# Optimization experiments

Measured on AMD Instinct MI355X. Metric: run time of the kernel, lower is better.

## Reference

```python
import jax, jax.numpy as jnp
import numpy as np


def setup_inputs() -> dict:
    key = jax.random.key(0)
    k = jax.random.split(key, 5)
    bs, n_heads, ch, n_obj, emb = 4, 8, 64, 8, 64
    ih = iw = 32
    T = ih * iw
    return {
        "qkv": jax.random.normal(k[0], (bs, 3 * n_heads * ch, T), dtype=jnp.float32),
        "bboxes": jax.random.uniform(k[1], (bs, n_obj, 5), dtype=jnp.float32),
        "null_prompt_emb": jax.random.normal(k[2], (bs, emb, T), dtype=jnp.float32),
        "prompt_emb": jax.random.normal(k[3], (bs, emb, T), dtype=jnp.float32),
        "W_prompt": jax.random.normal(k[4], (3 * n_heads * ch, emb), dtype=jnp.float32) * 0.02,
        "n_heads": n_heads,
        "image_h": ih,
        "image_w": iw,
    }


def _region_masks(bboxes, h, w):
    # Faithful translation of get_region: bbox unpacked as (x, y, width, height, obj_idx).
    # Returns float masks [b, n_obj, h*w].
    x, y, bw, bh = bboxes[..., 0], bboxes[..., 1], bboxes[..., 2], bboxes[..., 3]
    i0 = jnp.minimum(float(h) - 1.0, jnp.floor(y * h))
    j0 = jnp.minimum(float(w) - 1.0, jnp.floor(x * w))
    i1 = i0 + jnp.maximum(1.0, jnp.ceil(bh * h))
    j1 = j0 + jnp.maximum(1.0, jnp.ceil(bw * w))
    ii = jnp.arange(h, dtype=jnp.float32)
    jj = jnp.arange(w, dtype=jnp.float32)
    mi = (ii >= i0[..., None]) & (ii < i1[..., None])          # [b, n, h]
    mj = (jj >= j0[..., None]) & (jj < j1[..., None])          # [b, n, w]
    m = (mi[..., :, None] & mj[..., None, :]).astype(jnp.float32)  # [b, n, h, w]
    return m.reshape(m.shape[0], m.shape[1], h * w)


def reference(qkv, bboxes, null_prompt_emb, prompt_emb, W_prompt, n_heads, image_h, image_w):
    bs, width, T = qkv.shape
    ch = width // (3 * n_heads)
    scale = float(ch) ** -0.25  # 1/sqrt(sqrt(ch))

    def split3(x):
        x = x.reshape(bs * n_heads, 3 * ch, T)
        return x[:, :ch], x[:, ch:2 * ch], x[:, 2 * ch:]

    q, k, v = split3(qkv)
    # to_prompt_token is a 1x1 Conv1d (no bias) == matmul over the channel dim
    nq, nk, nv = split3(jnp.einsum('oc,bct->bot', W_prompt, null_prompt_emb))
    pq, pk, pv = split3(jnp.einsum('oc,bct->bot', W_prompt, prompt_emb))

    def attn(qh, kh, vh, col_mask=None):
        w = jnp.einsum('bct,bcs->bts', qh * scale, kh * scale)
        if col_mask is not None:
            w = jnp.where(col_mask[:, None, :] > 0.5, w, -1e9)
        w = jax.nn.softmax(w.astype(jnp.float32), axis=-1).astype(qh.dtype)
        return jnp.einsum('bts,bcs->btc', w, vh)  # [bs*heads, T, ch]

    # global (null-prompt) attention
    a_null = attn(q + nq, k + nk, v + nv)

    # per-object masked attention, blended by region masks
    masks = _region_masks(bboxes, image_h, image_w)       # [bs, n_obj, T]
    masks = jnp.repeat(masks, n_heads, axis=0)            # [(bs*heads), n_obj, T]
    qf, kf, vf = q + pq, k + pk, v + pv
    a_fg = jnp.zeros_like(a_null)
    counter = jnp.zeros((bs * n_heads, T, 1), dtype=jnp.float32)
    for o in range(masks.shape[1]):  # small fixed loop over objects
        m = masks[:, o]                                   # [bs*heads, T]
        a_fg = a_fg + m[:, :, None] * attn(qf, kf, vf, col_mask=m)
        counter = counter + m[:, :, None]
    fg = counter > 0.5
    a_final = jnp.where(fg, a_fg, a_null) / jnp.where(fg, counter, 1.0)
    return jnp.transpose(a_final, (0, 2, 1)).reshape(bs, n_heads * ch, T)
```

## Files before the change

kernel.cpp:

```cpp
#include <hip/hip_runtime.h>
#include <math.h>

#define BS 4
#define NH 8
#define TT 1024
#define WROWS 1536
#define NOBJ 8
#define NT 65536

#define QNT_OFF  0
#define KNT_OFF  2097152
#define VNCS_OFF 4194304
#define QFT_OFF  6291456
#define KFT_OFF  8388608
#define VFT_OFF  10485760

typedef __attribute__((ext_vector_type(8))) short short8;
typedef __attribute__((ext_vector_type(4))) float v4f;

#if __has_builtin(__builtin_amdgcn_exp2f)
#define EXP2(x) __builtin_amdgcn_exp2f(x)
#else
#define EXP2(x) exp2f(x)
#endif

__device__ __forceinline__ short f2bf(float f) {
    unsigned u = __float_as_uint(f);
    u = (u + 0x7FFF + ((u >> 16) & 1)) >> 16;
    return (short)u;
}
__device__ __forceinline__ unsigned p2(float a, float b) {
    return (unsigned)(unsigned short)f2bf(a) | ((unsigned)(unsigned short)f2bf(b) << 16);
}
__device__ __forceinline__ unsigned p2t(float a, float b) {
    return (__float_as_uint(a) >> 16) | (__float_as_uint(b) & 0xFFFF0000u);
}

__device__ __forceinline__ void get_region(const float* __restrict__ bb,
                                           int& i0, int& j0, int& hh, int& ww) {
    float x = bb[0], y = bb[1], bw = bb[2], bh = bb[3];
    float i0f = fminf(31.0f, floorf(y * 32.0f));
    float j0f = fminf(31.0f, floorf(x * 32.0f));
    float i1f = i0f + fmaxf(1.0f, ceilf(bh * 32.0f));
    float j1f = j0f + fmaxf(1.0f, ceilf(bw * 32.0f));
    i0 = (int)i0f; j0 = (int)j0f;
    int i1 = min(32, (int)i1f);
    int j1 = min(32, (int)j1f);
    hh = i1 - i0; ww = j1 - j0;
}

__global__ __launch_bounds__(256)
void fuse_kernel(const float* __restrict__ qkv, const float* __restrict__ nEmb,
                 const float* __restrict__ pEmb, const float* __restrict__ W,
                 short* __restrict__ wsS) {
    __shared__ float WtT[64][68];
    __shared__ float En[64][64];
    __shared__ float Ep[64][64];
    short* sbufA = (short*)&WtT[0][0];
    short* sbufB = (short*)&En[0][0];
    int t0 = blockIdx.x * 64;
    int r0 = blockIdx.y * 64;
    int b  = blockIdx.z;
    int tid = threadIdx.x;
    int half = tid >> 4;
    int q4 = (tid & 15) * 4;
    int tr = tid >> 4, tc = tid & 15;
    float4 xq[4];
#pragma unroll
    for (int i = 0; i < 4; ++i)
        xq[i] = *(const float4*)&qkv[(b * WROWS + r0 + tr * 4 + i) * TT + t0 + tc * 4];
#pragma unroll
    for (int p = 0; p < 4; ++p) {
        int rr = p * 16 + half;
        float4 w4 = *(const float4*)&W[(r0 + rr) * 64 + q4];
        WtT[q4 + 0][rr] = w4.x; WtT[q4 + 1][rr] = w4.y;
        WtT[q4 + 2][rr] = w4.z; WtT[q4 + 3][rr] = w4.w;
        int e = p * 16 + half;
        *(float4*)&En[e][q4] = *(const float4*)&nEmb[(b * 64 + e) * TT + t0 + q4];
        *(float4*)&Ep[e][q4] = *(const float4*)&pEmb[(b * 64 + e) * TT + t0 + q4];
    }
    __syncthreads();
    float an[4][4] = {{0.f}}, ap[4][4] = {{0.f}};
#pragma unroll 8
    for (int e = 0; e < 64; ++e) {
        float4 w4 = *(const float4*)&WtT[e][tr * 4];
        float4 n4 = *(const float4*)&En[e][tc * 4];
        float4 p4 = *(const float4*)&Ep[e][tc * 4];
        float w[4]  = {w4.x, w4.y, w4.z, w4.w};
        float nn[4] = {n4.x, n4.y, n4.z, n4.w};
        float pp[4] = {p4.x, p4.y, p4.z, p4.w};
#pragma unroll
        for (int i = 0; i < 4; ++i)
#pragma unroll
            for (int j = 0; j < 4; ++j) {
                an[i][j] += w[i] * nn[j];
                ap[i][j] += w[i] * pp[j];
            }
    }
    int sec = (r0 % 192) / 64;
    int h = r0 / 192, bh = b * 8 + h;
    float sc = (sec == 0) ? 0.18033688f : 1.0f;
#pragma unroll
    for (int i = 0; i < 4; ++i) {
        float4 x4 = xq[i];
        an[i][0] = (an[i][0] + x4.x) * sc; an[i][1] = (an[i][1] + x4.y) * sc;
        an[i][2] = (an[i][2] + x4.z) * sc; an[i][3] = (an[i][3] + x4.w) * sc;
        ap[i][0] = (ap[i][0] + x4.x) * sc; ap[i][1] = (ap[i][1] + x4.y) * sc;
        ap[i][2] = (ap[i][2] + x4.z) * sc; ap[i][3] = (ap[i][3] + x4.w) * sc;
    }
    if (sec == 2) {
        short* Vn = wsS + VNCS_OFF + bh * NT;
#pragma unroll
        for (int i = 0; i < 4; ++i) {
            int c = tr * 4 + i;
            uint2 pk; pk.x = p2(an[i][0], an[i][1]); pk.y = p2(an[i][2], an[i][3]);
            *(uint2*)&Vn[c * TT + t0 + tc * 4] = pk;
        }
        short* dst = wsS + VFT_OFF + bh * NT + t0 * 64;
        __syncthreads();
#pragma unroll
        for (int i = 0; i < 4; ++i)
#pragma unroll
            for (int j = 0; j < 4; ++j)
                sbufB[(tc * 4 + j) * 72 + tr * 4 + i] = f2bf(ap[i][j]);
        __syncthreads();
#pragma unroll
        for (int rep = 0; rep < 2; ++rep) {
            int idx = rep * 256 + tid; int tl = idx >> 3, c8 = idx & 7;
            *(short8*)&dst[tl * 64 + c8 * 8] = *(const short8*)&sbufB[tl * 72 + c8 * 8];
        }
    } else {
        short* dn = wsS + (sec == 0 ? QNT_OFF : KNT_OFF) + bh * NT + t0 * 64;
        short* df = wsS + (sec == 0 ? QFT_OFF : KFT_OFF) + bh * NT + t0 * 64;
        __syncthreads();
#pragma unroll
        for (int i = 0; i < 4; ++i)
#pragma unroll
            for (int j = 0; j < 4; ++j) {
                sbufA[(tc * 4 + j) * 72 + tr * 4 + i] = f2bf(an[i][j]);
                sbufB[(tc * 4 + j) * 72 + tr * 4 + i] = f2bf(ap[i][j]);
            }
        __syncthreads();
#pragma unroll
        for (int rep = 0; rep < 2; ++rep) {
            int idx = rep * 256 + tid; int tl = idx >> 3, c8 = idx & 7;
            *(short8*)&dn[tl * 64 + c8 * 8] = *(const short8*)&sbufA[tl * 72 + c8 * 8];
            *(short8*)&df[tl * 64 + c8 * 8] = *(const short8*)&sbufB[tl * 72 + c8 * 8];
        }
    }
}

__global__ __launch_bounds__(256)
void attn_fused(const short* __restrict__ wsS, const float* __restrict__ bboxes,
                float* __restrict__ out) {
    __shared__ __align__(16) short lds[13824];
    __shared__ unsigned short tmap[1024];
    short* Qs = lds;
    short* Ks = lds + 4608;
    short* Vs = lds + 9216;
    int bh = blockIdx.x, rt = blockIdx.y;
    int b = bh >> 3, h = bh & 7;
    int t0 = rt * 64;
    int tid = threadIdx.x;
    int w = tid >> 6, lane = tid & 63, ln = lane & 15, qd = lane >> 4;
    const short* QnT = wsS + QNT_OFF + bh * NT;
    const short* KnT = wsS + KNT_OFF + bh * NT;
    const short* Vn  = wsS + VNCS_OFF + bh * NT;
    const short* QfT = wsS + QFT_OFF + bh * NT;
    const short* KfT = wsS + KFT_OFF + bh * NT;
    const short* VfT = wsS + VFT_OFF + bh * NT;

    int r0i = 2 * rt, r1i = 2 * rt + 1;
    unsigned inter = 0u, cov0 = 0u, cov1 = 0u;
    for (int o = 0; o < NOBJ; ++o) {
        int i0, j0, hh, ww;
        get_region(&bboxes[(b * NOBJ + o) * 5], i0, j0, hh, ww);
        int i1 = i0 + hh;
        if (i0 <= r1i && i1 > r0i) {
            inter |= (1u << o);
            unsigned wm = (ww >= 32) ? 0xFFFFFFFFu : (((1u << ww) - 1u) << j0);
            if (i0 <= r0i && r0i < i1) cov0 |= wm;
            if (i0 <= r1i && r1i < i1) cov1 |= wm;
        }
    }

    v4f Onull[4];
#pragma unroll
    for (int cc = 0; cc < 4; ++cc) Onull[cc] = (v4f){0.f, 0.f, 0.f, 0.f};

    if ((cov0 & cov1) != 0xFFFFFFFFu) {
#pragma unroll
        for (int rep = 0; rep < 2; ++rep) {
            int idx = rep * 256 + tid; int cell = idx >> 3, o8 = idx & 7;
            *(short8*)&Qs[cell * 72 + o8 * 8] =
                *(const short8*)&QnT[(t0 + cell) * 64 + o8 * 8];
        }
        __syncthreads();
        short8 aq0 = *(const short8*)&Qs[(16 * w + ln) * 72 + qd * 8];
        short8 aq1 = *(const short8*)&Qs[(16 * w + ln) * 72 + 32 + qd * 8];
        v4f O[4]; float l[4];
#pragma unroll
        for (int r = 0; r < 4; ++r) l[r] = 0.f;
#pragma unroll
        for (int cc = 0; cc < 4; ++cc) O[cc] = (v4f){0.f, 0.f, 0.f, 0.f};
        short8 kreg[2], vreg[2];
#pragma unroll
        for (int rep = 0; rep < 2; ++rep) {
            int idx = rep * 256 + tid; int cell = idx >> 3, o8 = idx & 7;
            int pc = 4 * (cell & 15) + (cell >> 4);
            kreg[rep] = *(const short8*)&KnT[pc * 64 + o8 * 8];
            vreg[rep] = *(const short8*)&Vn[cell * TT + o8 * 8];
        }
        for (int ct = 0; ct < 16; ++ct) {
            __syncthreads();
#pragma unroll
            for (int rep = 0; rep < 2; ++rep) {
                int idx = rep * 256 + tid; int cell = idx >> 3, o8 = idx & 7;
                *(short8*)&Ks[cell * 72 + o8 * 8] = kreg[rep];
                *(short8*)&Vs[cell * 72 + o8 * 8] = vreg[rep];
            }
            __syncthreads();
            if (ct < 15) {
                int s0 = (ct + 1) * 64;
#pragma unroll
                for (int rep = 0; rep < 2; ++rep) {
                    int idx = rep * 256 + tid; int cell = idx >> 3, o8 = idx & 7;
                    int pc = 4 * (cell & 15) + (cell >> 4);
                    kreg[rep] = *(const short8*)&KnT[(s0 + pc) * 64 + o8 * 8];
                    vreg[rep] = *(const short8*)&Vn[cell * TT + s0 + o8 * 8];
                }
            }
            v4f S[4];
#pragma unroll
            for (int nn = 0; nn < 4; ++nn) {
                short8 b0 = *(const short8*)&Ks[(nn * 16 + ln) * 72 + qd * 8];
                short8 b1 = *(const short8*)&Ks[(nn * 16 + ln) * 72 + 32 + qd * 8];
                v4f z = (v4f){0.f, 0.f, 0.f, 0.f};
                z = __builtin_amdgcn_mfma_f32_16x16x32_bf16(aq0, b0, z, 0, 0, 0);
                z = __builtin_amdgcn_mfma_f32_16x16x32_bf16(aq1, b1, z, 0, 0, 0);
                S[nn] = z;
            }
#pragma unroll
            for (int r = 0; r < 4; ++r) {
                float e0 = EXP2(S[0][r]);
                float e1 = EXP2(S[1][r]);
                float e2 = EXP2(S[2][r]);
                float e3 = EXP2(S[3][r]);
                l[r] += e0 + e1 + e2 + e3;
                uint2 pk; pk.x = p2t(e0, e1); pk.y = p2t(e2, e3);
                *(uint2*)&Qs[(w * 16 + 4 * qd + r) * 72 + 4 * ln] = pk;
            }
            short8 ap0 = *(const short8*)&Qs[(w * 16 + ln) * 72 + qd * 8];
            short8 ap1 = *(const short8*)&Qs[(w * 16 + ln) * 72 + 32 + qd * 8];
#pragma unroll
            for (int cc = 0; cc < 4; ++cc) {
                short8 bv0 = *(const short8*)&Vs[(cc * 16 + ln) * 72 + qd * 8];
                short8 bv1 = *(const short8*)&Vs[(cc * 16 + ln) * 72 + 32 + qd * 8];
                O[cc] = __builtin_amdgcn_mfma_f32_16x16x32_bf16(ap0, bv0, O[cc], 0, 0, 0);
                O[cc] = __builtin_amdgcn_mfma_f32_16x16x32_bf16(ap1, bv1, O[cc], 0, 0, 0);
            }
        }
#pragma unroll
        for (int r = 0; r < 4; ++r) {
            float rs = l[r];
            rs += __shfl_xor(rs, 1, 64);
            rs += __shfl_xor(rs, 2, 64);
            rs += __shfl_xor(rs, 4, 64);
            rs += __shfl_xor(rs, 8, 64);
            float inv = 1.0f / rs;
#pragma unroll
            for (int cc = 0; cc < 4; ++cc) Onull[cc][r] = O[cc][r] * inv;
        }
    }

    v4f Oacc[4]; float cnt[4];
#pragma unroll
    for (int r = 0; r < 4; ++r) cnt[r] = 0.f;
#pragma unroll
    for (int cc = 0; cc < 4; ++cc) Oacc[cc] = (v4f){0.f, 0.f, 0.f, 0.f};

    if (inter != 0u) {
        __syncthreads();
#pragma unroll
        for (int rep = 0; rep < 2; ++rep) {
            int idx = rep * 256 + tid; int cell = idx >> 3, o8 = idx & 7;
            *(short8*)&Qs[cell * 72 + o8 * 8] =
                *(const short8*)&QfT[(t0 + cell) * 64 + o8 * 8];
        }
        __syncthreads();
        short8 aq0 = *(const short8*)&Qs[(16 * w + ln) * 72 + qd * 8];
        short8 aq1 = *(const short8*)&Qs[(16 * w + ln) * 72 + 32 + qd * 8];
        for (int o = 0; o < NOBJ; ++o) {
            if (!((inter >> o) & 1u)) continue;
            int i0, j0, hh, ww;
            get_region(&bboxes[(b * NOBJ + o) * 5], i0, j0, hh, ww);
            int i1 = i0 + hh;
            int R = hh * ww;
            for (int idx = tid; idx < R; idx += 256) {
                int ri = idx / ww; int rj = idx - ri * ww;
                tmap[idx] = (unsigned short)((i0 + ri) * 32 + j0 + rj);
            }
            __syncthreads();
            v4f O[4]; float l[4];
#pragma unroll
            for (int r = 0; r < 4; ++r) l[r] = 0.f;
#pragma unroll
            for (int cc = 0; cc < 4; ++cc) O[cc] = (v4f){0.f, 0.f, 0.f, 0.f};
            int nct = (R + 63) >> 6;
            short8 kreg[2], vreg[2];
#pragma unroll
            for (int rep = 0; rep < 2; ++rep) {
                int idx = rep * 256 + tid; int cell = idx >> 3, o8 = idx & 7;
                int pc = 4 * (cell & 15) + (cell >> 4);
                int tk = tmap[min(pc, R - 1)];
                int tv = tmap[min(cell, R - 1)];
                kreg[rep] = *(const short8*)&KfT[tk * 64 + o8 * 8];
                vreg[rep] = *(const short8*)&VfT[tv * 64 + o8 * 8];
            }
            for (int ct = 0; ct < nct; ++ct) {
                int sb = ct * 64;
                __syncthreads();
#pragma unroll
                for (int rep = 0; rep < 2; ++rep) {
                    int idx = rep * 256 + tid; int cell = idx >> 3, o8 = idx & 7;
                    *(short8*)&Ks[cell * 72 + o8 * 8] = kreg[rep];
#pragma unroll
                    for (int jj = 0; jj < 8; ++jj) {
                        int j = (jj + o8) & 7;
                        Vs[(o8 * 8 + j) * 72 + cell] = vreg[rep][j];
                    }
                }
                __syncthreads();
                if (ct + 1 < nct) {
                    int s0 = sb + 64;
#pragma unroll
                    for (int rep = 0; rep < 2; ++rep) {
                        int idx = rep * 256 + tid; int cell = idx >> 3, o8 = idx & 7;
                        int pc = 4 * (cell & 15) + (cell >> 4);
                        int tk = tmap[min(s0 + pc, R - 1)];
                        int tv = tmap[min(s0 + cell, R - 1)];
                        kreg[rep] = *(const short8*)&KfT[tk * 64 + o8 * 8];
                        vreg[rep] = *(const short8*)&VfT[tv * 64 + o8 * 8];
                    }
                }
                v4f S[4];
#pragma unroll
                for (int nn = 0; nn < 4; ++nn) {
                    short8 b0 = *(const short8*)&Ks[(nn * 16 + ln) * 72 + qd * 8];
                    short8 b1 = *(const short8*)&Ks[(nn * 16 + ln) * 72 + 32 + qd * 8];
                    v4f z = (v4f){0.f, 0.f, 0.f, 0.f};
                    z = __builtin_amdgcn_mfma_f32_16x16x32_bf16(aq0, b0, z, 0, 0, 0);
                    z = __builtin_amdgcn_mfma_f32_16x16x32_bf16(aq1, b1, z, 0, 0, 0);
                    S[nn] = z;
                }
                float v0 = (sb + 4 * ln + 0) < R ? 1.f : 0.f;
                float v1 = (sb + 4 * ln + 1) < R ? 1.f : 0.f;
                float v2 = (sb + 4 * ln + 2) < R ? 1.f : 0.f;
                float v3 = (sb + 4 * ln + 3) < R ? 1.f : 0.f;
#pragma unroll
                for (int r = 0; r < 4; ++r) {
                    float e0 = EXP2(S[0][r]) * v0;
                    float e1 = EXP2(S[1][r]) * v1;
                    float e2 = EXP2(S[2][r]) * v2;
                    float e3 = EXP2(S[3][r]) * v3;
                    l[r] += e0 + e1 + e2 + e3;
                    uint2 pk; pk.x = p2t(e0, e1); pk.y = p2t(e2, e3);
                    *(uint2*)&Qs[(w * 16 + 4 * qd + r) * 72 + 4 * ln] = pk;
                }
                short8 ap0 = *(const short8*)&Qs[(w * 16 + ln) * 72 + qd * 8];
                short8 ap1 = *(const short8*)&Qs[(w * 16 + ln) * 72 + 32 + qd * 8];
#pragma unroll
                for (int cc = 0; cc < 4; ++cc) {
                    short8 bv0 = *(const short8*)&Vs[(cc * 16 + ln) * 72 + qd * 8];
                    short8 bv1 = *(const short8*)&Vs[(cc * 16 + ln) * 72 + 32 + qd * 8];
                    O[cc] = __builtin_amdgcn_mfma_f32_16x16x32_bf16(ap0, bv0, O[cc], 0, 0, 0);
                    O[cc] = __builtin_amdgcn_mfma_f32_16x16x32_bf16(ap1, bv1, O[cc], 0, 0, 0);
                }
            }
#pragma unroll
            for (int r = 0; r < 4; ++r) {
                float rs = l[r];
                rs += __shfl_xor(rs, 1, 64);
                rs += __shfl_xor(rs, 2, 64);
                rs += __shfl_xor(rs, 4, 64);
                rs += __shfl_xor(rs, 8, 64);
                float inv = 1.0f / rs;
                int t = t0 + 16 * w + 4 * qd + r;
                int ti = t >> 5, tj = t & 31;
                bool in = (ti >= i0) && (ti < i1) && (tj >= j0) && (tj < j0 + ww);
                if (in) {
                    cnt[r] += 1.f;
#pragma unroll
                    for (int cc = 0; cc < 4; ++cc) Oacc[cc][r] += O[cc][r] * inv;
                }
            }
        }
    }

    __syncthreads();
    float* Ot = (float*)lds;
#pragma unroll
    for (int r = 0; r < 4; ++r) {
        int tl = 16 * w + 4 * qd + r;
        float icnt = cnt[r] > 0.f ? 1.0f / cnt[r] : 0.f;
#pragma unroll
        for (int cc = 0; cc < 4; ++cc) {
            float val = cnt[r] > 0.f ? Oacc[cc][r] * icnt : Onull[cc][r];
            Ot[(cc * 16 + ln) * 68 + tl] = val;
        }
    }
    __syncthreads();
    int obase = (b * 512 + h * 64) * TT + t0;
#pragma unroll
    for (int rep = 0; rep < 4; ++rep) {
        int idx = rep * 256 + tid; int c = idx >> 4, t4 = (idx & 15) * 4;
        *(float4*)&out[obase + c * TT + t4] = *(float4*)&Ot[c * 68 + t4];
    }
}

extern "C" void kernel_launch(void* const* d_in, const int* in_sizes, int n_in,
                              void* d_out, int out_size, void* d_ws, size_t ws_size,
                              hipStream_t stream) {
    const float* qkv    = (const float*)d_in[0];
    const float* bboxes = (const float*)d_in[1];
    const float* nEmb   = (const float*)d_in[2];
    const float* pEmb   = (const float*)d_in[3];
    const float* W      = (const float*)d_in[4];
    short* wsS = (short*)d_ws;
    float* out = (float*)d_out;

    fuse_kernel<<<dim3(16, 24, 4), 256, 0, stream>>>(qkv, nEmb, pEmb, W, wsS);
    attn_fused<<<dim3(32, 16), 256, 0, stream>>>(wsS, bboxes, out);
}
```

Before: 162.1 us.

## Compute null attention only for uncovered tokens via compacted token list

Adds a small kernel that builds, per batch, a compacted list of tokens not covered by any bbox. A new kernel runs null-prompt attention only for those query rows, in 16-row tiles with the key range split across four waves and a reduction through shared memory. The foreground kernel no longer computes null attention and writes only covered tokens. This drops null attention for covered rows (previously done for any 64-row tile with an uncovered token), at the cost of two extra launches, scattered output stores and gathered query loads.

```diff
diff --git a/kernel.cpp b/kernel.cpp
--- a/kernel.cpp
+++ b/kernel.cpp
@@ -14,6 +14,8 @@
 #define QFT_OFF  6291456
 #define KFT_OFF  8388608
 #define VFT_OFF  10485760
+#define ULIST_OFF 12582912
+#define UCNT_BYTE_OFF 25174016
 
 typedef __attribute__((ext_vector_type(8))) short short8;
 typedef __attribute__((ext_vector_type(4))) float v4f;
@@ -47,6 +49,48 @@
     int i1 = min(32, (int)i1f);
     int j1 = min(32, (int)j1f);
     hh = i1 - i0; ww = j1 - j0;
+}
+
+__global__ __launch_bounds__(256)
+void list_kernel(const float* __restrict__ bboxes,
+                 unsigned short* __restrict__ ulist, int* __restrict__ ucnt) {
+    int b = blockIdx.x, tid = threadIdx.x;
+    int I0[NOBJ], I1[NOBJ], J0[NOBJ], J1[NOBJ];
+#pragma unroll
+    for (int o = 0; o < NOBJ; ++o) {
+        int i0, j0, hh, ww;
+        get_region(&bboxes[(b * NOBJ + o) * 5], i0, j0, hh, ww);
+        I0[o] = i0; I1[o] = i0 + hh; J0[o] = j0; J1[o] = j0 + ww;
+    }
+    int u[4], uc = 0;
+#pragma unroll
+    for (int j = 0; j < 4; ++j) {
+        int t = tid * 4 + j, ti = t >> 5, tj = t & 31;
+        bool cov = false;
+#pragma unroll
+        for (int o = 0; o < NOBJ; ++o)
+            cov = cov || (ti >= I0[o] && ti < I1[o] && tj >= J0[o] && tj < J1[o]);
+        u[j] = cov ? 0 : 1; uc += u[j];
+    }
+    int lane = tid & 63, w = tid >> 6;
+    int s = uc;
+#pragma unroll
+    for (int d = 1; d < 64; d <<= 1) {
+        int v = __shfl_up(s, d, 64);
+        if (lane >= d) s += v;
+    }
+    __shared__ int wsum[4];
+    if (lane == 63) wsum[w] = s;
+    __syncthreads();
+    int off = 0;
+    for (int i = 0; i < w; ++i) off += wsum[i];
+    int base = off + s - uc;
+    int k = 0;
+#pragma unroll
+    for (int j = 0; j < 4; ++j) {
+        if (u[j]) { ulist[b * 1024 + base + k] = (unsigned short)(tid * 4 + j); ++k; }
+    }
+    if (tid == 0) ucnt[b] = wsum[0] + wsum[1] + wsum[2] + wsum[3];
 }
 
 __global__ __launch_bounds__(256)
@@ -151,8 +195,117 @@
 }
 
 __global__ __launch_bounds__(256)
-void attn_fused(const short* __restrict__ wsS, const float* __restrict__ bboxes,
-                float* __restrict__ out) {
+void attn_null_u(const short* __restrict__ wsS,
+                 const unsigned short* __restrict__ ulist,
+                 const int* __restrict__ ucnt, float* __restrict__ out) {
+    __shared__ __align__(16) short Ps[4 * 1152];
+    __shared__ float Rbuf[3][64][20];
+    int bh = blockIdx.x, rt = blockIdx.y;
+    int b = bh >> 3, h = bh & 7;
+    int U = ucnt[b];
+    int n0 = rt * 16;
+    if (n0 >= U) return;
+    int tid = threadIdx.x;
+    int w = tid >> 6, lane = tid & 63, ln = lane & 15, qd = lane >> 4;
+    const short* QnT = wsS + QNT_OFF + bh * NT;
+    const short* KnT = wsS + KNT_OFF + bh * NT;
+    const short* Vn  = wsS + VNCS_OFF + bh * NT;
+    const unsigned short* ul = ulist + b * 1024;
+    int trow = ul[min(n0 + ln, U - 1)];
+    short8 aq0 = *(const short8*)&QnT[trow * 64 + qd * 8];
+    short8 aq1 = *(const short8*)&QnT[trow * 64 + 32 + qd * 8];
+    v4f O[4]; float l[4];
+#pragma unroll
+    for (int r = 0; r < 4; ++r) l[r] = 0.f;
+#pragma unroll
+    for (int cc = 0; cc < 4; ++cc) O[cc] = (v4f){0.f, 0.f, 0.f, 0.f};
+    short* Pw = Ps + w * 1152;
+#pragma unroll
+    for (int i = 0; i < 4; ++i) {
+        int s0 = (w * 4 + i) * 64;
+        short8 kf[4][2], vf[4][2];
+#pragma unroll
+        for (int nn = 0; nn < 4; ++nn) {
+            int base = (s0 + 4 * ln + nn) * 64;
+            kf[nn][0] = *(const short8*)&KnT[base + qd * 8];
+            kf[nn][1] = *(const short8*)&KnT[base + 32 + qd * 8];
+        }
+#pragma unroll
+        for (int cc = 0; cc < 4; ++cc) {
+            int base = (cc * 16 + ln) * TT + s0;
+            vf[cc][0] = *(const short8*)&Vn[base + qd * 8];
+            vf[cc][1] = *(const short8*)&Vn[base + 32 + qd * 8];
+        }
+        v4f S[4];
+#pragma unroll
+        for (int nn = 0; nn < 4; ++nn) {
+            v4f z = (v4f){0.f, 0.f, 0.f, 0.f};
+            z = __builtin_amdgcn_mfma_f32_16x16x32_bf16(aq0, kf[nn][0], z, 0, 0, 0);
+            z = __builtin_amdgcn_mfma_f32_16x16x32_bf16(aq1, kf[nn][1], z, 0, 0, 0);
+            S[nn] = z;
+        }
+#pragma unroll
+        for (int r = 0; r < 4; ++r) {
+            float e0 = EXP2(S[0][r]);
+            float e1 = EXP2(S[1][r]);
+            float e2 = EXP2(S[2][r]);
+            float e3 = EXP2(S[3][r]);
+            l[r] += e0 + e1 + e2 + e3;
+            uint2 pk; pk.x = p2t(e0, e1); pk.y = p2t(e2, e3);
+            *(uint2*)&Pw[(qd * 4 + r) * 72 + 4 * ln] = pk;
+        }
+        short8 ap0 = *(const short8*)&Pw[ln * 72 + qd * 8];
+        short8 ap1 = *(const short8*)&Pw[ln * 72 + 32 + qd * 8];
+#pragma unroll
+        for (int cc = 0; cc < 4; ++cc) {
+            O[cc] = __builtin_amdgcn_mfma_f32_16x16x32_bf16(ap0, vf[cc][0], O[cc], 0, 0, 0);
+            O[cc] = __builtin_amdgcn_mfma_f32_16x16x32_bf16(ap1, vf[cc][1], O[cc], 0, 0, 0);
+        }
+    }
+#pragma unroll
+    for (int r = 0; r < 4; ++r) {
+        l[r] += __shfl_xor(l[r], 1, 64);
+        l[r] += __shfl_xor(l[r], 2, 64);
+        l[r] += __shfl_xor(l[r], 4, 64);
+        l[r] += __shfl_xor(l[r], 8, 64);
+    }
+    if (w > 0) {
+#pragma unroll
+        for (int cc = 0; cc < 4; ++cc)
+#pragma unroll
+            for (int r = 0; r < 4; ++r) Rbuf[w - 1][lane][cc * 4 + r] = O[cc][r];
+#pragma unroll
+        for (int r = 0; r < 4; ++r) Rbuf[w - 1][lane][16 + r] = l[r];
+    }
+    __syncthreads();
+    if (w == 0) {
+#pragma unroll
+        for (int ww = 0; ww < 3; ++ww) {
+#pragma unroll
+            for (int cc = 0; cc < 4; ++cc)
+#pragma unroll
+                for (int r = 0; r < 4; ++r) O[cc][r] += Rbuf[ww][lane][cc * 4 + r];
+#pragma unroll
+            for (int r = 0; r < 4; ++r) l[r] += Rbuf[ww][lane][16 + r];
+        }
+        int obase = (b * 512 + h * 64) * TT;
+#pragma unroll
+        for (int r = 0; r < 4; ++r) {
+            int rank = n0 + qd * 4 + r;
+            if (rank < U) {
+                int t = ul[rank];
+                float inv = 1.0f / l[r];
+#pragma unroll
+                for (int cc = 0; cc < 4; ++cc)
+                    out[obase + (cc * 16 + ln) * TT + t] = O[cc][r] * inv;
+            }
+        }
+    }
+}
+
+__global__ __launch_bounds__(256)
+void attn_fg(const short* __restrict__ wsS, const float* __restrict__ bboxes,
+             float* __restrict__ out) {
     __shared__ __align__(16) short lds[13824];
     __shared__ unsigned short tmap[1024];
     short* Qs = lds;
@@ -163,9 +316,6 @@
     int t0 = rt * 64;
     int tid = threadIdx.x;
     int w = tid >> 6, lane = tid & 63, ln = lane & 15, qd = lane >> 4;
-    const short* QnT = wsS + QNT_OFF + bh * NT;
-    const short* KnT = wsS + KNT_OFF + bh * NT;
-    const short* Vn  = wsS + VNCS_OFF + bh * NT;
     const short* QfT = wsS + QFT_OFF + bh * NT;
     const short* KfT = wsS + KFT_OFF + bh * NT;
     const short* VfT = wsS + VFT_OFF + bh * NT;
@@ -183,51 +333,74 @@
             if (i0 <= r1i && r1i < i1) cov1 |= wm;
         }
     }
-
-    v4f Onull[4];
-#pragma unroll
-    for (int cc = 0; cc < 4; ++cc) Onull[cc] = (v4f){0.f, 0.f, 0.f, 0.f};
-
-    if ((cov0 & cov1) != 0xFFFFFFFFu) {
-#pragma unroll
-        for (int rep = 0; rep < 2; ++rep) {
-            int idx = rep * 256 + tid; int cell = idx >> 3, o8 = idx & 7;
-            *(short8*)&Qs[cell * 72 + o8 * 8] =
-                *(const short8*)&QnT[(t0 + cell) * 64 + o8 * 8];
+    if (inter == 0u) return;
+
+#pragma unroll
+    for (int rep = 0; rep < 2; ++rep) {
+        int idx = rep * 256 + tid; int cell = idx >> 3, o8 = idx & 7;
+        *(short8*)&Qs[cell * 72 + o8 * 8] =
+            *(const short8*)&QfT[(t0 + cell) * 64 + o8 * 8];
+    }
+    __syncthreads();
+    short8 aq0 = *(const short8*)&Qs[(16 * w + ln) * 72 + qd * 8];
+    short8 aq1 = *(const short8*)&Qs[(16 * w + ln) * 72 + 32 + qd * 8];
+    v4f Oacc[4]; float cnt[4];
+#pragma unroll
+    for (int r = 0; r < 4; ++r) cnt[r] = 0.f;
+#pragma unroll
+    for (int cc = 0; cc < 4; ++cc) Oacc[cc] = (v4f){0.f, 0.f, 0.f, 0.f};
+
+    for (int o = 0; o < NOBJ; ++o) {
+        if (!((inter >> o) & 1u)) continue;
+        int i0, j0, hh, ww;
+        get_region(&bboxes[(b * NOBJ + o) * 5], i0, j0, hh, ww);
+        int i1 = i0 + hh;
+        int R = hh * ww;
+        for (int idx = tid; idx < R; idx += 256) {
+            int ri = idx / ww; int rj = idx - ri * ww;
+            tmap[idx] = (unsigned short)((i0 + ri) * 32 + j0 + rj);
         }
         __syncthreads();
-        short8 aq0 = *(const short8*)&Qs[(16 * w + ln) * 72 + qd * 8];
-        short8 aq1 = *(const short8*)&Qs[(16 * w + ln) * 72 + 32 + qd * 8];
         v4f O[4]; float l[4];
 #pragma unroll
         for (int r = 0; r < 4; ++r) l[r] = 0.f;
 #pragma unroll
         for (int cc = 0; cc < 4; ++cc) O[cc] = (v4f){0.f, 0.f, 0.f, 0.f};
+        int nct = (R + 63) >> 6;
         short8 kreg[2], vreg[2];
 #pragma unroll
         for (int rep = 0; rep < 2; ++rep) {
             int idx = rep * 256 + tid; int cell = idx >> 3, o8 = idx & 7;
             int pc = 4 * (cell & 15) + (cell >> 4);
-            kreg[rep] = *(const short8*)&KnT[pc * 64 + o8 * 8];
-            vreg[rep] = *(const short8*)&Vn[cell * TT + o8 * 8];
-        }
-        for (int ct = 0; ct < 16; ++ct) {
+            int tk = tmap[min(pc, R - 1)];
+            int tv = tmap[min(cell, R - 1)];
+            kreg[rep] = *(const short8*)&KfT[tk * 64 + o8 * 8];
+            vreg[rep] = *(const short8*)&VfT[tv * 64 + o8 * 8];
+        }
+        for (int ct = 0; ct < nct; ++ct) {
+            int sb = ct * 64;
             __syncthreads();
 #pragma unroll
             for (int rep = 0; rep < 2; ++rep) {
                 int idx = rep * 256 + tid; int cell = idx >> 3, o8 = idx & 7;
                 *(short8*)&Ks[cell * 72 + o8 * 8] = kreg[rep];
-                *(short8*)&Vs[cell * 72 + o8 * 8] = vreg[rep];
+#pragma unroll
+                for (int jj = 0; jj < 8; ++jj) {
+                    int j = (jj + o8) & 7;
+                    Vs[(o8 * 8 + j) * 72 + cell] = vreg[rep][j];
+                }
             }
             __syncthreads();
-            if (ct < 15) {
-                int s0 = (ct + 1) * 64;
+            if (ct + 1 < nct) {
+                int s0 = sb + 64;
 #pragma unroll
                 for (int rep = 0; rep < 2; ++rep) {
                     int idx = rep * 256 + tid; int cell = idx >> 3, o8 = idx & 7;
                     int pc = 4 * (cell & 15) + (cell >> 4);
-                    kreg[rep] = *(const short8*)&KnT[(s0 + pc) * 64 + o8 * 8];
-                    vreg[rep] = *(const short8*)&Vn[cell * TT + s0 + o8 * 8];
+                    int tk = tmap[min(s0 + pc, R - 1)];
+                    int tv = tmap[min(s0 + cell, R - 1)];
+                    kreg[rep] = *(const short8*)&KfT[tk * 64 + o8 * 8];
+                    vreg[rep] = *(const short8*)&VfT[tv * 64 + o8 * 8];
                 }
             }
             v4f S[4];
@@ -240,12 +413,16 @@
                 z = __builtin_amdgcn_mfma_f32_16x16x32_bf16(aq1, b1, z, 0, 0, 0);
                 S[nn] = z;
             }
+            float v0 = (sb + 4 * ln + 0) < R ? 1.f : 0.f;
+            float v1 = (sb + 4 * ln + 1) < R ? 1.f : 0.f;
+            float v2 = (sb + 4 * ln + 2) < R ? 1.f : 0.f;
+            float v3 = (sb + 4 * ln + 3) < R ? 1.f : 0.f;
 #pragma unroll
             for (int r = 0; r < 4; ++r) {
-                float e0 = EXP2(S[0][r]);
-                float e1 = EXP2(S[1][r]);
-                float e2 = EXP2(S[2][r]);
-                float e3 = EXP2(S[3][r]);
+                float e0 = EXP2(S[0][r]) * v0;
+                float e1 = EXP2(S[1][r]) * v1;
+                float e2 = EXP2(S[2][r]) * v2;
+                float e3 = EXP2(S[3][r]) * v3;
                 l[r] += e0 + e1 + e2 + e3;
                 uint2 pk; pk.x = p2t(e0, e1); pk.y = p2t(e2, e3);
                 *(uint2*)&Qs[(w * 16 + 4 * qd + r) * 72 + 4 * ln] = pk;
@@ -268,131 +445,13 @@
             rs += __shfl_xor(rs, 4, 64);
             rs += __shfl_xor(rs, 8, 64);
             float inv = 1.0f / rs;
-#pragma unroll
-            for (int cc = 0; cc < 4; ++cc) Onull[cc][r] = O[cc][r] * inv;
-        }
-    }
-
-    v4f Oacc[4]; float cnt[4];
-#pragma unroll
-    for (int r = 0; r < 4; ++r) cnt[r] = 0.f;
-#pragma unroll
-    for (int cc = 0; cc < 4; ++cc) Oacc[cc] = (v4f){0.f, 0.f, 0.f, 0.f};
-
-    if (inter != 0u) {
-        __syncthreads();
-#pragma unroll
-        for (int rep = 0; rep < 2; ++rep) {
-            int idx = rep * 256 + tid; int cell = idx >> 3, o8 = idx & 7;
-            *(short8*)&Qs[cell * 72 + o8 * 8] =
-                *(const short8*)&QfT[(t0 + cell) * 64 + o8 * 8];
-        }
-        __syncthreads();
-        short8 aq0 = *(const short8*)&Qs[(16 * w + ln) * 72 + qd * 8];
-        short8 aq1 = *(const short8*)&Qs[(16 * w + ln) * 72 + 32 + qd * 8];
-        for (int o = 0; o < NOBJ; ++o) {
-            if (!((inter >> o) & 1u)) continue;
-            int i0, j0, hh, ww;
-            get_region(&bboxes[(b * NOBJ + o) * 5], i0, j0, hh, ww);
-            int i1 = i0 + hh;
-            int R = hh * ww;
-            for (int idx = tid; idx < R; idx += 256) {
-                int ri = idx / ww; int rj = idx - ri * ww;
-                tmap[idx] = (unsigned short)((i0 + ri) * 32 + j0 + rj);
-            }
-            __syncthreads();
-            v4f O[4]; float l[4];
-#pragma unroll
-            for (int r = 0; r < 4; ++r) l[r] = 0.f;
-#pragma unroll
-            for (int cc = 0; cc < 4; ++cc) O[cc] = (v4f){0.f, 0.f, 0.f, 0.f};
-            int nct = (R + 63) >> 6;
-            short8 kreg[2], vreg[2];
-#pragma unroll
-            for (int rep = 0; rep < 2; ++rep) {
-                int idx = rep * 256 + tid; int cell = idx >> 3, o8 = idx & 7;
-                int pc = 4 * (cell & 15) + (cell >> 4);
-                int tk = tmap[min(pc, R - 1)];
-                int tv = tmap[min(cell, R - 1)];
-                kreg[rep] = *(const short8*)&KfT[tk * 64 + o8 * 8];
-                vreg[rep] = *(const short8*)&VfT[tv * 64 + o8 * 8];
-            }
-            for (int ct = 0; ct < nct; ++ct) {
-                int sb = ct * 64;
-                __syncthreads();
-#pragma unroll
-                for (int rep = 0; rep < 2; ++rep) {
-                    int idx = rep * 256 + tid; int cell = idx >> 3, o8 = idx & 7;
-                    *(short8*)&Ks[cell * 72 + o8 * 8] = kreg[rep];
-#pragma unroll
-                    for (int jj = 0; jj < 8; ++jj) {
-                        int j = (jj + o8) & 7;
-                        Vs[(o8 * 8 + j) * 72 + cell] = vreg[rep][j];
-                    }
-                }
-                __syncthreads();
-                if (ct + 1 < nct) {
-                    int s0 = sb + 64;
-#pragma unroll
-                    for (int rep = 0; rep < 2; ++rep) {
-                        int idx = rep * 256 + tid; int cell = idx >> 3, o8 = idx & 7;
-                        int pc = 4 * (cell & 15) + (cell >> 4);
-                        int tk = tmap[min(s0 + pc, R - 1)];
-                        int tv = tmap[min(s0 + cell, R - 1)];
-                        kreg[rep] = *(const short8*)&KfT[tk * 64 + o8 * 8];
-                        vreg[rep] = *(const short8*)&VfT[tv * 64 + o8 * 8];
-                    }
-                }
-                v4f S[4];
-#pragma unroll
-                for (int nn = 0; nn < 4; ++nn) {
-                    short8 b0 = *(const short8*)&Ks[(nn * 16 + ln) * 72 + qd * 8];
-                    short8 b1 = *(const short8*)&Ks[(nn * 16 + ln) * 72 + 32 + qd * 8];
-                    v4f z = (v4f){0.f, 0.f, 0.f, 0.f};
-                    z = __builtin_amdgcn_mfma_f32_16x16x32_bf16(aq0, b0, z, 0, 0, 0);
-                    z = __builtin_amdgcn_mfma_f32_16x16x32_bf16(aq1, b1, z, 0, 0, 0);
-                    S[nn] = z;
-                }
-                float v0 = (sb + 4 * ln + 0) < R ? 1.f : 0.f;
-                float v1 = (sb + 4 * ln + 1) < R ? 1.f : 0.f;
-                float v2 = (sb + 4 * ln + 2) < R ? 1.f : 0.f;
-                float v3 = (sb + 4 * ln + 3) < R ? 1.f : 0.f;
-#pragma unroll
-                for (int r = 0; r < 4; ++r) {
-                    float e0 = EXP2(S[0][r]) * v0;
-                    float e1 = EXP2(S[1][r]) * v1;
-                    float e2 = EXP2(S[2][r]) * v2;
-                    float e3 = EXP2(S[3][r]) * v3;
-                    l[r] += e0 + e1 + e2 + e3;
-                    uint2 pk; pk.x = p2t(e0, e1); pk.y = p2t(e2, e3);
-                    *(uint2*)&Qs[(w * 16 + 4 * qd + r) * 72 + 4 * ln] = pk;
-                }
-                short8 ap0 = *(const short8*)&Qs[(w * 16 + ln) * 72 + qd * 8];
-                short8 ap1 = *(const short8*)&Qs[(w * 16 + ln) * 72 + 32 + qd * 8];
-#pragma unroll
-                for (int cc = 0; cc < 4; ++cc) {
-                    short8 bv0 = *(const short8*)&Vs[(cc * 16 + ln) * 72 + qd * 8];
-                    short8 bv1 = *(const short8*)&Vs[(cc * 16 + ln) * 72 + 32 + qd * 8];
-                    O[cc] = __builtin_amdgcn_mfma_f32_16x16x32_bf16(ap0, bv0, O[cc], 0, 0, 0);
-                    O[cc] = __builtin_amdgcn_mfma_f32_16x16x32_bf16(ap1, bv1, O[cc], 0, 0, 0);
-                }
-            }
-#pragma unroll
-            for (int r = 0; r < 4; ++r) {
-                float rs = l[r];
-                rs += __shfl_xor(rs, 1, 64);
-                rs += __shfl_xor(rs, 2, 64);
-                rs += __shfl_xor(rs, 4, 64);
-                rs += __shfl_xor(rs, 8, 64);
-                float inv = 1.0f / rs;
-                int t = t0 + 16 * w + 4 * qd + r;
-                int ti = t >> 5, tj = t & 31;
-                bool in = (ti >= i0) && (ti < i1) && (tj >= j0) && (tj < j0 + ww);
-                if (in) {
-                    cnt[r] += 1.f;
-#pragma unroll
-                    for (int cc = 0; cc < 4; ++cc) Oacc[cc][r] += O[cc][r] * inv;
-                }
+            int t = t0 + 16 * w + 4 * qd + r;
+            int ti = t >> 5, tj = t & 31;
+            bool in = (ti >= i0) && (ti < i1) && (tj >= j0) && (tj < j0 + ww);
+            if (in) {
+                cnt[r] += 1.f;
+#pragma unroll
+                for (int cc = 0; cc < 4; ++cc) Oacc[cc][r] += O[cc][r] * inv;
             }
         }
     }
@@ -404,17 +463,21 @@
         int tl = 16 * w + 4 * qd + r;
         float icnt = cnt[r] > 0.f ? 1.0f / cnt[r] : 0.f;
 #pragma unroll
-        for (int cc = 0; cc < 4; ++cc) {
-            float val = cnt[r] > 0.f ? Oacc[cc][r] * icnt : Onull[cc][r];
-            Ot[(cc * 16 + ln) * 68 + tl] = val;
-        }
+        for (int cc = 0; cc < 4; ++cc)
+            Ot[(cc * 16 + ln) * 68 + tl] = Oacc[cc][r] * icnt;
     }
     __syncthreads();
     int obase = (b * 512 + h * 64) * TT + t0;
 #pragma unroll
     for (int rep = 0; rep < 4; ++rep) {
         int idx = rep * 256 + tid; int c = idx >> 4, t4 = (idx & 15) * 4;
-        *(float4*)&out[obase + c * TT + t4] = *(float4*)&Ot[c * 68 + t4];
+#pragma unroll
+        for (int j = 0; j < 4; ++j) {
+            int tl = t4 + j;
+            unsigned cv = (tl < 32) ? cov0 : cov1;
+            if ((cv >> (tl & 31)) & 1u)
+                out[obase + c * TT + tl] = Ot[c * 68 + tl];
+        }
     }
 }
 
@@ -427,8 +490,12 @@
     const float* pEmb   = (const float*)d_in[3];
     const float* W      = (const float*)d_in[4];
     short* wsS = (short*)d_ws;
+    unsigned short* ulist = (unsigned short*)(wsS + ULIST_OFF);
+    int* ucntp = (int*)((char*)d_ws + UCNT_BYTE_OFF);
     float* out = (float*)d_out;
 
+    list_kernel<<<4, 256, 0, stream>>>(bboxes, ulist, ucntp);
     fuse_kernel<<<dim3(16, 24, 4), 256, 0, stream>>>(qkv, nEmb, pEmb, W, wsS);
-    attn_fused<<<dim3(32, 16), 256, 0, stream>>>(wsS, bboxes, out);
-}
+    attn_null_u<<<dim3(32, 64), 256, 0, stream>>>(wsS, ulist, ucntp, out);
+    attn_fg<<<dim3(32, 16), 256, 0, stream>>>(wsS, bboxes, out);
+}
```

After: 188.0 us. 16.0% more time.

## Split null and foreground attention into separate blocks via grid z dimension

Applied to the files above, without the earlier changes.

The fused attention kernel now launches twice as many blocks. Blocks with z=0 compute the per-object masked foreground attention and write only the covered positions. Blocks with z=1 compute the global null-prompt attention and write only the uncovered positions. This raises parallelism and shortens the per-block critical path, since the null and foreground phases previously ran back to back in one block. The cost is redundant bbox and coverage computation per block and scalar, uncoalesced masked stores in place of float4 stores.

```diff
diff --git a/kernel.cpp b/kernel.cpp
--- a/kernel.cpp
+++ b/kernel.cpp
@@ -151,24 +151,18 @@
 }
 
 __global__ __launch_bounds__(256)
-void attn_fused(const short* __restrict__ wsS, const float* __restrict__ bboxes,
+void attn_split(const short* __restrict__ wsS, const float* __restrict__ bboxes,
                 float* __restrict__ out) {
     __shared__ __align__(16) short lds[13824];
     __shared__ unsigned short tmap[1024];
     short* Qs = lds;
     short* Ks = lds + 4608;
     short* Vs = lds + 9216;
-    int bh = blockIdx.x, rt = blockIdx.y;
+    int bh = blockIdx.x, rt = blockIdx.y, phase = blockIdx.z;
     int b = bh >> 3, h = bh & 7;
     int t0 = rt * 64;
     int tid = threadIdx.x;
     int w = tid >> 6, lane = tid & 63, ln = lane & 15, qd = lane >> 4;
-    const short* QnT = wsS + QNT_OFF + bh * NT;
-    const short* KnT = wsS + KNT_OFF + bh * NT;
-    const short* Vn  = wsS + VNCS_OFF + bh * NT;
-    const short* QfT = wsS + QFT_OFF + bh * NT;
-    const short* KfT = wsS + KFT_OFF + bh * NT;
-    const short* VfT = wsS + VFT_OFF + bh * NT;
 
     int r0i = 2 * rt, r1i = 2 * rt + 1;
     unsigned inter = 0u, cov0 = 0u, cov1 = 0u;
@@ -183,104 +177,13 @@
             if (i0 <= r1i && r1i < i1) cov1 |= wm;
         }
     }
-
-    v4f Onull[4];
-#pragma unroll
-    for (int cc = 0; cc < 4; ++cc) Onull[cc] = (v4f){0.f, 0.f, 0.f, 0.f};
-
-    if ((cov0 & cov1) != 0xFFFFFFFFu) {
-#pragma unroll
-        for (int rep = 0; rep < 2; ++rep) {
-            int idx = rep * 256 + tid; int cell = idx >> 3, o8 = idx & 7;
-            *(short8*)&Qs[cell * 72 + o8 * 8] =
-                *(const short8*)&QnT[(t0 + cell) * 64 + o8 * 8];
-        }
-        __syncthreads();
-        short8 aq0 = *(const short8*)&Qs[(16 * w + ln) * 72 + qd * 8];
-        short8 aq1 = *(const short8*)&Qs[(16 * w + ln) * 72 + 32 + qd * 8];
-        v4f O[4]; float l[4];
-#pragma unroll
-        for (int r = 0; r < 4; ++r) l[r] = 0.f;
-#pragma unroll
-        for (int cc = 0; cc < 4; ++cc) O[cc] = (v4f){0.f, 0.f, 0.f, 0.f};
-        short8 kreg[2], vreg[2];
-#pragma unroll
-        for (int rep = 0; rep < 2; ++rep) {
-            int idx = rep * 256 + tid; int cell = idx >> 3, o8 = idx & 7;
-            int pc = 4 * (cell & 15) + (cell >> 4);
-            kreg[rep] = *(const short8*)&KnT[pc * 64 + o8 * 8];
-            vreg[rep] = *(const short8*)&Vn[cell * TT + o8 * 8];
-        }
-        for (int ct = 0; ct < 16; ++ct) {
-            __syncthreads();
-#pragma unroll
-            for (int rep = 0; rep < 2; ++rep) {
-                int idx = rep * 256 + tid; int cell = idx >> 3, o8 = idx & 7;
-                *(short8*)&Ks[cell * 72 + o8 * 8] = kreg[rep];
-                *(short8*)&Vs[cell * 72 + o8 * 8] = vreg[rep];
-            }
-            __syncthreads();
-            if (ct < 15) {
-                int s0 = (ct + 1) * 64;
-#pragma unroll
-                for (int rep = 0; rep < 2; ++rep) {
-                    int idx = rep * 256 + tid; int cell = idx >> 3, o8 = idx & 7;
-                    int pc = 4 * (cell & 15) + (cell >> 4);
-                    kreg[rep] = *(const short8*)&KnT[(s0 + pc) * 64 + o8 * 8];
-                    vreg[rep] = *(const short8*)&Vn[cell * TT + s0 + o8 * 8];
-                }
-            }
-            v4f S[4];
-#pragma unroll
-            for (int nn = 0; nn < 4; ++nn) {
-                short8 b0 = *(const short8*)&Ks[(nn * 16 + ln) * 72 + qd * 8];
-                short8 b1 = *(const short8*)&Ks[(nn * 16 + ln) * 72 + 32 + qd * 8];
-                v4f z = (v4f){0.f, 0.f, 0.f, 0.f};
-                z = __builtin_amdgcn_mfma_f32_16x16x32_bf16(aq0, b0, z, 0, 0, 0);
-                z = __builtin_amdgcn_mfma_f32_16x16x32_bf16(aq1, b1, z, 0, 0, 0);
-                S[nn] = z;
-            }
-#pragma unroll
-            for (int r = 0; r < 4; ++r) {
-                float e0 = EXP2(S[0][r]);
-                float e1 = EXP2(S[1][r]);
-                float e2 = EXP2(S[2][r]);
-                float e3 = EXP2(S[3][r]);
-                l[r] += e0 + e1 + e2 + e3;
-                uint2 pk; pk.x = p2t(e0, e1); pk.y = p2t(e2, e3);
-                *(uint2*)&Qs[(w * 16 + 4 * qd + r) * 72 + 4 * ln] = pk;
-            }
-            short8 ap0 = *(const short8*)&Qs[(w * 16 + ln) * 72 + qd * 8];
-            short8 ap1 = *(const short8*)&Qs[(w * 16 + ln) * 72 + 32 + qd * 8];
-#pragma unroll
-            for (int cc = 0; cc < 4; ++cc) {
-                short8 bv0 = *(const short8*)&Vs[(cc * 16 + ln) * 72 + qd * 8];
-                short8 bv1 = *(const short8*)&Vs[(cc * 16 + ln) * 72 + 32 + qd * 8];
-                O[cc] = __builtin_amdgcn_mfma_f32_16x16x32_bf16(ap0, bv0, O[cc], 0, 0, 0);
-                O[cc] = __builtin_amdgcn_mfma_f32_16x16x32_bf16(ap1, bv1, O[cc], 0, 0, 0);
-            }
-        }
-#pragma unroll
-        for (int r = 0; r < 4; ++r) {
-            float rs = l[r];
-            rs += __shfl_xor(rs, 1, 64);
-            rs += __shfl_xor(rs, 2, 64);
-            rs += __shfl_xor(rs, 4, 64);
-            rs += __shfl_xor(rs, 8, 64);
-            float inv = 1.0f / rs;
-#pragma unroll
-            for (int cc = 0; cc < 4; ++cc) Onull[cc][r] = O[cc][r] * inv;
-        }
-    }
-
-    v4f Oacc[4]; float cnt[4];
-#pragma unroll
-    for (int r = 0; r < 4; ++r) cnt[r] = 0.f;
-#pragma unroll
-    for (int cc = 0; cc < 4; ++cc) Oacc[cc] = (v4f){0.f, 0.f, 0.f, 0.f};
-
-    if (inter != 0u) {
-        __syncthreads();
+    int obase = (b * 512 + h * 64) * TT + t0;
+
+    if (phase == 0) {
+        if (inter == 0u) return;
+        const short* QfT = wsS + QFT_OFF + bh * NT;
+        const short* KfT = wsS + KFT_OFF + bh * NT;
+        const short* VfT = wsS + VFT_OFF + bh * NT;
 #pragma unroll
         for (int rep = 0; rep < 2; ++rep) {
             int idx = rep * 256 + tid; int cell = idx >> 3, o8 = idx & 7;
@@ -290,6 +193,12 @@
         __syncthreads();
         short8 aq0 = *(const short8*)&Qs[(16 * w + ln) * 72 + qd * 8];
         short8 aq1 = *(const short8*)&Qs[(16 * w + ln) * 72 + 32 + qd * 8];
+        v4f Oacc[4]; float cnt[4];
+#pragma unroll
+        for (int r = 0; r < 4; ++r) cnt[r] = 0.f;
+#pragma unroll
+        for (int cc = 0; cc < 4; ++cc) Oacc[cc] = (v4f){0.f, 0.f, 0.f, 0.f};
+
         for (int o = 0; o < NOBJ; ++o) {
             if (!((inter >> o) & 1u)) continue;
             int i0, j0, hh, ww;
@@ -395,26 +304,136 @@
                 }
             }
         }
-    }
-
-    __syncthreads();
-    float* Ot = (float*)lds;
-#pragma unroll
-    for (int r = 0; r < 4; ++r) {
-        int tl = 16 * w + 4 * qd + r;
-        float icnt = cnt[r] > 0.f ? 1.0f / cnt[r] : 0.f;
-#pragma unroll
-        for (int cc = 0; cc < 4; ++cc) {
-            float val = cnt[r] > 0.f ? Oacc[cc][r] * icnt : Onull[cc][r];
-            Ot[(cc * 16 + ln) * 68 + tl] = val;
-        }
-    }
-    __syncthreads();
-    int obase = (b * 512 + h * 64) * TT + t0;
-#pragma unroll
-    for (int rep = 0; rep < 4; ++rep) {
-        int idx = rep * 256 + tid; int c = idx >> 4, t4 = (idx & 15) * 4;
-        *(float4*)&out[obase + c * TT + t4] = *(float4*)&Ot[c * 68 + t4];
+        __syncthreads();
+        float* Ot = (float*)lds;
+#pragma unroll
+        for (int r = 0; r < 4; ++r) {
+            int tl = 16 * w + 4 * qd + r;
+            float icnt = cnt[r] > 0.f ? 1.0f / cnt[r] : 0.f;
+#pragma unroll
+            for (int cc = 0; cc < 4; ++cc)
+                Ot[(cc * 16 + ln) * 68 + tl] = Oacc[cc][r] * icnt;
+        }
+        __syncthreads();
+#pragma unroll
+        for (int rep = 0; rep < 4; ++rep) {
+            int idx = rep * 256 + tid; int c = idx >> 4, t4 = (idx & 15) * 4;
+#pragma unroll
+            for (int j = 0; j < 4; ++j) {
+                int tl = t4 + j;
+                unsigned cv = (tl < 32) ? cov0 : cov1;
+                if ((cv >> (tl & 31)) & 1u)
+                    out[obase + c * TT + tl] = Ot[c * 68 + tl];
+            }
+        }
+    } else {
+        if ((cov0 & cov1) == 0xFFFFFFFFu) return;
+        const short* QnT = wsS + QNT_OFF + bh * NT;
+        const short* KnT = wsS + KNT_OFF + bh * NT;
+        const short* Vn  = wsS + VNCS_OFF + bh * NT;
+#pragma unroll
+        for (int rep = 0; rep < 2; ++rep) {
+            int idx = rep * 256 + tid; int cell = idx >> 3, o8 = idx & 7;
+            *(short8*)&Qs[cell * 72 + o8 * 8] =
+                *(const short8*)&QnT[(t0 + cell) * 64 + o8 * 8];
+        }
+        __syncthreads();
+        short8 aq0 = *(const short8*)&Qs[(16 * w + ln) * 72 + qd * 8];
+        short8 aq1 = *(const short8*)&Qs[(16 * w + ln) * 72 + 32 + qd * 8];
+        v4f O[4]; float l[4];
+#pragma unroll
+        for (int r = 0; r < 4; ++r) l[r] = 0.f;
+#pragma unroll
+        for (int cc = 0; cc < 4; ++cc) O[cc] = (v4f){0.f, 0.f, 0.f, 0.f};
+        short8 kreg[2], vreg[2];
+#pragma unroll
+        for (int rep = 0; rep < 2; ++rep) {
+            int idx = rep * 256 + tid; int cell = idx >> 3, o8 = idx & 7;
+            int pc = 4 * (cell & 15) + (cell >> 4);
+            kreg[rep] = *(const short8*)&KnT[pc * 64 + o8 * 8];
+            vreg[rep] = *(const short8*)&Vn[cell * TT + o8 * 8];
+        }
+        for (int ct = 0; ct < 16; ++ct) {
+            __syncthreads();
+#pragma unroll
+            for (int rep = 0; rep < 2; ++rep) {
+                int idx = rep * 256 + tid; int cell = idx >> 3, o8 = idx & 7;
+                *(short8*)&Ks[cell * 72 + o8 * 8] = kreg[rep];
+                *(short8*)&Vs[cell * 72 + o8 * 8] = vreg[rep];
+            }
+            __syncthreads();
+            if (ct < 15) {
+                int s0 = (ct + 1) * 64;
+#pragma unroll
+                for (int rep = 0; rep < 2; ++rep) {
+                    int idx = rep * 256 + tid; int cell = idx >> 3, o8 = idx & 7;
+                    int pc = 4 * (cell & 15) + (cell >> 4);
+                    kreg[rep] = *(const short8*)&KnT[(s0 + pc) * 64 + o8 * 8];
+                    vreg[rep] = *(const short8*)&Vn[cell * TT + s0 + o8 * 8];
+                }
+            }
+            v4f S[4];
+#pragma unroll
+            for (int nn = 0; nn < 4; ++nn) {
+                short8 b0 = *(const short8*)&Ks[(nn * 16 + ln) * 72 + qd * 8];
+                short8 b1 = *(const short8*)&Ks[(nn * 16 + ln) * 72 + 32 + qd * 8];
+                v4f z = (v4f){0.f, 0.f, 0.f, 0.f};
+                z = __builtin_amdgcn_mfma_f32_16x16x32_bf16(aq0, b0, z, 0, 0, 0);
+                z = __builtin_amdgcn_mfma_f32_16x16x32_bf16(aq1, b1, z, 0, 0, 0);
+                S[nn] = z;
+            }
+#pragma unroll
+            for (int r = 0; r < 4; ++r) {
+                float e0 = EXP2(S[0][r]);
+                float e1 = EXP2(S[1][r]);
+                float e2 = EXP2(S[2][r]);
+                float e3 = EXP2(S[3][r]);
+                l[r] += e0 + e1 + e2 + e3;
+                uint2 pk; pk.x = p2t(e0, e1); pk.y = p2t(e2, e3);
+                *(uint2*)&Qs[(w * 16 + 4 * qd + r) * 72 + 4 * ln] = pk;
+            }
+            short8 ap0 = *(const short8*)&Qs[(w * 16 + ln) * 72 + qd * 8];
+            short8 ap1 = *(const short8*)&Qs[(w * 16 + ln) * 72 + 32 + qd * 8];
+#pragma unroll
+            for (int cc = 0; cc < 4; ++cc) {
+                short8 bv0 = *(const short8*)&Vs[(cc * 16 + ln) * 72 + qd * 8];
+                short8 bv1 = *(const short8*)&Vs[(cc * 16 + ln) * 72 + 32 + qd * 8];
+                O[cc] = __builtin_amdgcn_mfma_f32_16x16x32_bf16(ap0, bv0, O[cc], 0, 0, 0);
+                O[cc] = __builtin_amdgcn_mfma_f32_16x16x32_bf16(ap1, bv1, O[cc], 0, 0, 0);
+            }
+        }
+#pragma unroll
+        for (int r = 0; r < 4; ++r) {
+            float rs = l[r];
+            rs += __shfl_xor(rs, 1, 64);
+            rs += __shfl_xor(rs, 2, 64);
+            rs += __shfl_xor(rs, 4, 64);
+            rs += __shfl_xor(rs, 8, 64);
+            float inv = 1.0f / rs;
+#pragma unroll
+            for (int cc = 0; cc < 4; ++cc) O[cc][r] *= inv;
+        }
+        __syncthreads();
+        float* Ot = (float*)lds;
+#pragma unroll
+        for (int r = 0; r < 4; ++r) {
+            int tl = 16 * w + 4 * qd + r;
+#pragma unroll
+            for (int cc = 0; cc < 4; ++cc)
+                Ot[(cc * 16 + ln) * 68 + tl] = O[cc][r];
+        }
+        __syncthreads();
+#pragma unroll
+        for (int rep = 0; rep < 4; ++rep) {
+            int idx = rep * 256 + tid; int c = idx >> 4, t4 = (idx & 15) * 4;
+#pragma unroll
+            for (int j = 0; j < 4; ++j) {
+                int tl = t4 + j;
+                unsigned cv = (tl < 32) ? cov0 : cov1;
+                if (!((cv >> (tl & 31)) & 1u))
+                    out[obase + c * TT + tl] = Ot[c * 68 + tl];
+            }
+        }
     }
 }
 
@@ -430,5 +449,5 @@
     float* out = (float*)d_out;
 
     fuse_kernel<<<dim3(16, 24, 4), 256, 0, stream>>>(qkv, nEmb, pEmb, W, wsS);
-    attn_fused<<<dim3(32, 16), 256, 0, stream>>>(wsS, bboxes, out);
-}
+    attn_split<<<dim3(32, 16, 2), 256, 0, stream>>>(wsS, bboxes, out);
+}
```

New measurement: 161.2 us. Within noise of the previous version (-0.5%).
